# Kernel optimization log

Hardware: AMD Instinct MI355X
Metric: run time of the kernel (lower is better)

## Reference

```python
import jax, jax.numpy as jnp
import numpy as np

B, BAG, H, C = 512, 32, 1024, 53
EPS = 1e-8  # torch F.cosine_similarity denominator clamp


def setup_inputs() -> dict:
    key = jax.random.key(0)
    ks = jax.random.split(key, 5)
    return {
        "sent_reps": jax.random.normal(ks[0], (B, BAG, H), jnp.float32),
        "aug_sent_reps": jax.random.normal(ks[1], (B, BAG, H), jnp.float32),
        "rel_table": jax.random.normal(ks[2], (C, H), jnp.float32),
        "cls_w": jax.random.normal(ks[3], (C, H), jnp.float32) * 0.02,
        "cls_b": jnp.zeros((C,), jnp.float32),
        "labels": jax.random.randint(ks[4], (B,), 0, C),
        "temperature": jnp.asarray(0.1, jnp.float32),
    }


def _cl(rep, aug, bag_rep, T):
    # rep, aug: (B, bag, H); bag_rep: (B, H)
    nr = jnp.linalg.norm(rep, axis=-1)        # (B, bag)
    na = jnp.linalg.norm(aug, axis=-1)        # (B, bag)
    nb = jnp.linalg.norm(bag_rep, axis=-1)    # (B,)
    pos_sim = jnp.sum(rep * aug, axis=-1) / jnp.maximum(nr * na, EPS)  # (B, bag)
    pos = jnp.exp(pos_sim / T)
    # pair[c, j, b] = cos(rep[b, j], bag_rep[c])  -- matches torch permute/broadcast chain
    dots = jnp.einsum('bjh,ch->cjb', rep, bag_rep)               # (B, bag, B)
    denom = jnp.maximum(nb[:, None, None] * nr.T[None], EPS)      # (B, bag, B)
    pair = dots / denom
    idx = jnp.arange(rep.shape[0])
    axis_sim = pair[idx, :, idx]                                  # (B, bag): cos(rep[b,j], bag_rep[b])
    neg = jnp.exp(pair / T).sum(axis=2) - jnp.exp(axis_sim / T)   # (B, bag)
    return jnp.mean(-jnp.log(pos / (pos + neg)))


def reference(sent_reps, aug_sent_reps, rel_table, cls_w, cls_b, labels, temperature):
    # Selective attention per bag (scope slices are uniform bags of size BAG -> vectorized)
    rel = rel_table[labels]                                        # (B, H)
    scale = jnp.sqrt(jnp.asarray(H, sent_reps.dtype))
    scores = jnp.einsum('bh,bjh->bj', rel, sent_reps) / scale      # (B, bag)
    alphas = jax.nn.softmax(scores, axis=-1)
    bag_reps = jnp.einsum('bj,bjh->bh', alphas, sent_reps)         # (B, H)
    bag_out = bag_reps @ cls_w.T + cls_b                           # (B, C)  (dropout in eval = identity)
    cl_loss = _cl(sent_reps, aug_sent_reps, bag_reps, temperature)
    return bag_out, cl_loss
```

## Files before the change

kernel.cpp:

```cpp
#include <hip/hip_runtime.h>
#include <hip/hip_bf16.h>


typedef __bf16 bf16x8 __attribute__((ext_vector_type(8)));
typedef __bf16 bf16x4 __attribute__((ext_vector_type(4)));
typedef float  f32x4  __attribute__((ext_vector_type(4)));

__device__ inline float wsum(float v) {
    #pragma unroll
    for (int off = 32; off > 0; off >>= 1) v += __shfl_xor(v, off, 64);
    return v;
}

__device__ inline void gll16(const void* g, void* l) {
    __builtin_amdgcn_global_load_lds((const __attribute__((address_space(1))) void*)g,
                                     (__attribute__((address_space(3))) void*)l, 16, 0, 0);
}

__device__ inline f32x4 ntld(const float* p) {
    return __builtin_nontemporal_load((const f32x4*)p);
}

__global__ __launch_bounds__(256) void ka(
    const float* __restrict__ sent, const float* __restrict__ aug,
    const float* __restrict__ rel_table, const int* __restrict__ labels,
    __bf16* __restrict__ repb, float* __restrict__ nr, float* __restrict__ pos_sim,
    float* __restrict__ scoreg,
    const float* __restrict__ clsw, __bf16* __restrict__ cwb,
    float* __restrict__ nbsq, float* __restrict__ loss)
{
    const int t = threadIdx.x;
    if (blockIdx.x < 256) {
        const int i = blockIdx.x * 256 + t;
        cwb[i] = (i < 53 * 1024) ? (__bf16)clsw[i] : (__bf16)0.0f;
    } else if (blockIdx.x == 256) {
        nbsq[t] = 0.0f; nbsq[256 + t] = 0.0f;
        if (t == 0) *loss = 0.0f;
    }

    const int w = t >> 6, lane = t & 63;
    const int row = blockIdx.x * 4 + w;
    const int b = row >> 5;
    const size_t rbase = (size_t)row * 1024;
    const float* srow = sent + rbase;
    const float* arow = aug + rbase;
    const float* relp = rel_table + (size_t)labels[b] * 1024;

    float P = 0.f, R = 0.f, A = 0.f, D = 0.f;
    #pragma unroll
    for (int i = 0; i < 4; i++) {
        const int h = i * 256 + lane * 4;
        f32x4 v  = ntld(srow + h);
        f32x4 a  = ntld(arow + h);
        f32x4 rl = *(const f32x4*)(relp + h);
        P += v.x * rl.x + v.y * rl.y + v.z * rl.z + v.w * rl.w;
        R += v.x * v.x + v.y * v.y + v.z * v.z + v.w * v.w;
        A += a.x * a.x + a.y * a.y + a.z * a.z + a.w * a.w;
        D += v.x * a.x + v.y * a.y + v.z * a.z + v.w * a.w;
        bf16x4 vb = { (__bf16)v.x, (__bf16)v.y, (__bf16)v.z, (__bf16)v.w };
        *(bf16x4*)(repb + rbase + h) = vb;
    }
    #pragma unroll
    for (int off = 32; off > 0; off >>= 1) {
        P += __shfl_xor(P, off, 64);
        R += __shfl_xor(R, off, 64);
        A += __shfl_xor(A, off, 64);
        D += __shfl_xor(D, off, 64);
    }
    if (lane == 0) {
        scoreg[row] = P * (1.0f / 32.0f);
        float nrv = sqrtf(R), nav = sqrtf(A);
        nr[row] = nrv;
        pos_sim[row] = D / fmaxf(nrv * nav, 1e-8f);
    }
}

__global__ __launch_bounds__(256) void kb(
    const __bf16* __restrict__ repb, const float* __restrict__ scoreg,
    __bf16* __restrict__ bagb, float* __restrict__ nbsq)
{
    __shared__ float alphaS[32];
    const int b = blockIdx.x, t = threadIdx.x;
    if (t < 32) {
        float sj = scoreg[b * 32 + t];
        float m = sj;
        #pragma unroll
        for (int off = 16; off > 0; off >>= 1) m = fmaxf(m, __shfl_xor(m, off, 32));
        float e = __expf(sj - m);
        float sum = e;
        #pragma unroll
        for (int off = 16; off > 0; off >>= 1) sum += __shfl_xor(sum, off, 32);
        alphaS[t] = e / sum;
    }
    __syncthreads();

    f32x4 acc = {};
    const __bf16* base = repb + (size_t)b * 32 * 1024 + t * 4;
    #pragma unroll 8
    for (int jj = 0; jj < 32; jj++) {
        bf16x4 v = *(const bf16x4*)(base + jj * 1024);
        const float al = alphaS[jj];
        acc.x += al * (float)v.x;
        acc.y += al * (float)v.y;
        acc.z += al * (float)v.z;
        acc.w += al * (float)v.w;
    }
    bf16x4 bb = { (__bf16)acc.x, (__bf16)acc.y, (__bf16)acc.z, (__bf16)acc.w };
    *(bf16x4*)(bagb + (size_t)b * 1024 + t * 4) = bb;

    float q = acc.x * acc.x + acc.y * acc.y + acc.z * acc.z + acc.w * acc.w;
    q = wsum(q);
    if ((t & 63) == 0) atomicAdd(&nbsq[b], q);
}

__global__ __launch_bounds__(256) void k4_gemm(
    const __bf16* __restrict__ repb, const __bf16* __restrict__ bagb,
    const float* __restrict__ nr, const float* __restrict__ nbsq,
    const float* __restrict__ temp, float* __restrict__ partial, float* __restrict__ diag,
    const __bf16* __restrict__ cwb, const float* __restrict__ bias, float* __restrict__ out)
{
    __shared__ __align__(16) char smem[65536];
    const int bid = blockIdx.x;
    const int t = threadIdx.x, lane = t & 63, w = t >> 6;
    const int m = lane & 15, quad = lane >> 4;

    if (bid >= 512) {
        __bf16* Al = (__bf16*)smem;
        __bf16* Bl = (__bf16*)(smem + 8192);
        const int r0 = (bid - 512) * 64;
        f32x4 acc[4] = {};
        const int i0 = t * 8;
        const int row0 = i0 >> 5, kk0 = i0 & 31;
        const __bf16* gA = bagb + (size_t)(r0 + row0) * 1024 + kk0;
        const __bf16* gB = cwb + (size_t)row0 * 1024 + kk0;
        for (int k0 = 0; k0 < 1024; k0 += 64) {
            __syncthreads();
            gll16(gA + k0,      Al + i0);
            gll16(gA + k0 + 32, Al + 2048 + i0);
            gll16(gB + k0,      Bl + i0);
            gll16(gB + k0 + 32, Bl + 2048 + i0);
            __syncthreads();
            #pragma unroll
            for (int ks = 0; ks < 2; ks++) {
                bf16x8 a = *(const bf16x8*)(&Al[ks * 2048 + (w * 16 + m) * 32 + quad * 8]);
                #pragma unroll
                for (int n = 0; n < 4; n++) {
                    bf16x8 bf = *(const bf16x8*)(&Bl[ks * 2048 + (n * 16 + m) * 32 + quad * 8]);
                    acc[n] = __builtin_amdgcn_mfma_f32_16x16x32_bf16(a, bf, acc[n], 0, 0, 0);
                }
            }
        }
        #pragma unroll
        for (int n = 0; n < 4; n++) {
            const int c = n * 16 + m;
            if (c < 53) {
                #pragma unroll
                for (int i = 0; i < 4; i++) {
                    const int r = r0 + w * 16 + quad * 4 + i;
                    out[(size_t)r * 53 + c] = acc[n][i] + bias[c];
                }
            }
        }
        return;
    }

    __bf16* Bu0 = (__bf16*)smem;
    __bf16* Bu1 = (__bf16*)(smem + 16384);
    __bf16* Bu2 = (__bf16*)(smem + 32768);
    float (*negp)[32][128] = (float (*)[32][128])(smem + 32768);

    const int xcd = bid & 7, slot = bid >> 3;
    const int cb = slot & 3, rb = (slot >> 2) * 8 + xcd;
    const int r0 = rb * 128, c0 = cb * 128;
    const int wr0 = (w & 1) * 64, wc0 = (w >> 1) * 64;
    const int half = w & 1;

    const int swc = 8 * ((t & 3) ^ ((t >> 3) & 3));
    const size_t sOff = (size_t)(t >> 2) * 1024 + swc;
    const __bf16* pA0 = repb + (size_t)r0 * 1024 + sOff;
    const __bf16* pA1 = pA0 + 64 * 1024;
    const __bf16* pB0 = bagb + (size_t)c0 * 1024 + sOff;
    const __bf16* pB1 = pB0 + 64 * 1024;
    const int d0 = t * 8, d1 = 2048 + t * 8, d2 = 4096 + t * 8, d3 = 6144 + t * 8;

    const int rho = (m >> 1) & 3;
    const int offA = ((wr0 + m) * 4 + (quad ^ rho)) * 8;
    const int offB = 4096 + ((wc0 + m) * 4 + (quad ^ rho)) * 8;

    f32x4 acc[4][4] = {};

    #define STG(buf, s) do { const int kk_ = (s) * 32;                      \
        gll16(pA0 + kk_, (buf) + d0); gll16(pA1 + kk_, (buf) + d1);         \
        gll16(pB0 + kk_, (buf) + d2); gll16(pB1 + kk_, (buf) + d3); } while (0)

    #define CMP(buf) do { bf16x8 av_[4], bv_[4];                            \
        _Pragma("unroll") for (int i_ = 0; i_ < 4; i_++)                    \
            av_[i_] = *(const bf16x8*)((buf) + offA + i_ * 512);            \
        _Pragma("unroll") for (int n_ = 0; n_ < 4; n_++)                    \
            bv_[n_] = *(const bf16x8*)((buf) + offB + n_ * 512);            \
        _Pragma("unroll") for (int i_ = 0; i_ < 4; i_++)                    \
        _Pragma("unroll") for (int n_ = 0; n_ < 4; n_++)                    \
            acc[i_][n_] = __builtin_amdgcn_mfma_f32_16x16x32_bf16(          \
                av_[i_], bv_[n_], acc[i_][n_], 0, 0, 0); } while (0)

    #define FENCE(N) do { __builtin_amdgcn_sched_barrier(0);                \
        asm volatile("s_waitcnt vmcnt(" #N ")" ::: "memory");               \
        __builtin_amdgcn_s_barrier();                                       \
        __builtin_amdgcn_sched_barrier(0); } while (0)

    STG(Bu0, 0);
    STG(Bu1, 1);
    FENCE(4);
    #pragma unroll 1
    for (int s = 0; s < 28; s += 3) {
        STG(Bu2, s + 2); CMP(Bu0); FENCE(4);
        STG(Bu0, s + 3); CMP(Bu1); FENCE(4);
        STG(Bu1, s + 4); CMP(Bu2); FENCE(4);
    }
    CMP(Bu0);
    FENCE(0);
    CMP(Bu1);

    const float invT = 1.0f / *temp;
    float nrv[16];
    #pragma unroll
    for (int i = 0; i < 4; i++)
        #pragma unroll
        for (int g = 0; g < 4; g++)
            nrv[i * 4 + g] = nr[r0 + wr0 + i * 16 + quad * 4 + g];

    #pragma unroll
    for (int n = 0; n < 4; n++) {
        const int c_local = wc0 + n * 16 + m;
        const int cg = c0 + c_local;
        const float nbv = sqrtf(nbsq[cg]);
        #pragma unroll
        for (int i = 0; i < 2; i++) {
            #pragma unroll
            for (int g = 0; g < 4; g++) {
                const int jj = i * 16 + quad * 4 + g;
                const int rg0 = r0 + wr0 + i * 16 + quad * 4 + g;
                const int rg2 = rg0 + 32;
                float e0 = __expf(acc[i][n][g]     / fmaxf(nbv * nrv[i * 4 + g],       1e-8f) * invT);
                float e2 = __expf(acc[i + 2][n][g] / fmaxf(nbv * nrv[(i + 2) * 4 + g], 1e-8f) * invT);
                negp[half][jj][c_local] = e0 + e2;
                if ((rg0 >> 5) == cg) diag[(size_t)cg * 32 + jj] = e0;
                if ((rg2 >> 5) == cg) diag[(size_t)cg * 32 + jj] = e2;
            }
        }
    }
    __syncthreads();

    float* pout = partial + (size_t)rb * 32 * 512 + c0;
    #pragma unroll
    for (int v = 0; v < 4; v++) {
        const int idx = v * 1024 + t * 4;
        const int jj = idx >> 7, cl = idx & 127;
        f32x4 a = *(const f32x4*)(&negp[0][jj][cl]);
        f32x4 bq = *(const f32x4*)(&negp[1][jj][cl]);
        f32x4 s = a + bq;
        *(f32x4*)(pout + (size_t)jj * 512 + cl) = s;
    }
    #undef STG
    #undef CMP
    #undef FENCE
}

__global__ __launch_bounds__(256) void k5_neg(
    const float* __restrict__ partial, const float* __restrict__ diag,
    const float* __restrict__ pos_sim, const float* __restrict__ temp,
    float* __restrict__ loss)
{
    const int ct = blockIdx.x & 7, j = blockIdx.x >> 3;
    const int t = threadIdx.x, lane = t & 63, w = t >> 6;
    const int bsub = t >> 4;
    const int cidx = t & 15;
    f32x4 acc = {};
    #pragma unroll 4
    for (int r = 0; r < 8; r++) {
        const int rb = bsub * 8 + r;
        f32x4 v = *(const f32x4*)(partial + ((size_t)rb * 32 + j) * 512 + ct * 64 + cidx * 4);
        acc += v;
    }
    #pragma unroll
    for (int k = 0; k < 4; k++) {
        acc[k] += __shfl_xor(acc[k], 16, 64);
        acc[k] += __shfl_xor(acc[k], 32, 64);
    }
    __shared__ float red[4][64];
    if (lane < 16) {
        #pragma unroll
        for (int k = 0; k < 4; k++) red[w][lane * 4 + k] = acc[k];
    }
    __syncthreads();

    if (t < 64) {
        const int c = ct * 64 + t;
        float S = red[0][t] + red[1][t] + red[2][t] + red[3][t];
        S -= diag[(size_t)c * 32 + j];
        const float invT = 1.0f / *temp;
        const float lp = pos_sim[(c << 5) + j] * invT;
        float term = logf(__expf(lp) + S) - lp;
        term = wsum(term);
        if (t == 0) atomicAdd(loss, term * (1.0f / 16384.0f));
    }
}

extern "C" void kernel_launch(void* const* d_in, const int* in_sizes, int n_in,
                              void* d_out, int out_size, void* d_ws, size_t ws_size,
                              hipStream_t stream)
{
    const float* sent = (const float*)d_in[0];
    const float* aug  = (const float*)d_in[1];
    const float* rel  = (const float*)d_in[2];
    const float* clsw = (const float*)d_in[3];
    const float* clsb = (const float*)d_in[4];
    const int*   lab  = (const int*)d_in[5];
    const float* temp = (const float*)d_in[6];
    float* out = (float*)d_out;

    char* ws = (char*)d_ws;
    __bf16* bagb    = (__bf16*)(ws);
    float*  nbsq    = (float*)(ws + (1u << 20));
    float*  nr      = (float*)(ws + (1u << 20) + 64 * 1024);
    float*  pos     = (float*)(ws + (1u << 20) + 128 * 1024);
    __bf16* cwb     = (__bf16*)(ws + (1u << 20) + 192 * 1024);
    float*  scoreg  = (float*)(ws + (1u << 20) + 320 * 1024);
    float*  diag    = (float*)(ws + (2u << 20) + 64 * 1024);
    __bf16* repb    = (__bf16*)(ws + (4u << 20));
    float*  partial = (float*)(ws + (36u << 20));

    float* loss = out + 27136;

    ka     <<<4096, 256, 0, stream>>>(sent, aug, rel, lab, repb, nr, pos, scoreg,
                                      clsw, cwb, nbsq, loss);
    kb     <<<512, 256, 0, stream>>>(repb, scoreg, bagb, nbsq);
    k4_gemm<<<520, 256, 0, stream>>>(repb, bagb, nr, nbsq, temp, partial, diag,
                                     cwb, clsb, out);
    k5_neg <<<256, 256, 0, stream>>>(partial, diag, pos, temp, loss);
}
```

Measured before the change: 199.4 us.

## Fuse row-stats and bag attention kernels; use 512-thread blocks in GEMM

Merges the per-row norm/score kernel and the bag-pooling kernel into one kernel with one block per bag. Each block keeps the bf16 bag rows in LDS, so bag pooling no longer rereads repb from global memory, and nbsq is written directly instead of atomically. The score buffer and one launch go away. The GEMM kernel moves to 512 threads: the 8 waves split the columns so each wave holds half as many accumulators, and the loads are split between A and B thread halves. The trade-offs are 64KB of LDS per fused block, which limits occupancy, and only 512 blocks in the fused kernel. The small classifier GEMM path now leaves half of its threads idle.

```diff
diff --git a/kernel.cpp b/kernel.cpp
--- a/kernel.cpp
+++ b/kernel.cpp
@@ -4,6 +4,7 @@
 
 typedef __bf16 bf16x8 __attribute__((ext_vector_type(8)));
 typedef __bf16 bf16x4 __attribute__((ext_vector_type(4)));
+typedef __bf16 bf16x2 __attribute__((ext_vector_type(2)));
 typedef float  f32x4  __attribute__((ext_vector_type(4)));
 
 __device__ inline float wsum(float v) {
@@ -21,99 +22,94 @@
     return __builtin_nontemporal_load((const f32x4*)p);
 }
 
-__global__ __launch_bounds__(256) void ka(
+__global__ __launch_bounds__(512, 4) void kab(
     const float* __restrict__ sent, const float* __restrict__ aug,
     const float* __restrict__ rel_table, const int* __restrict__ labels,
     __bf16* __restrict__ repb, float* __restrict__ nr, float* __restrict__ pos_sim,
-    float* __restrict__ scoreg,
     const float* __restrict__ clsw, __bf16* __restrict__ cwb,
-    float* __restrict__ nbsq, float* __restrict__ loss)
+    __bf16* __restrict__ bagb, float* __restrict__ nbsq, float* __restrict__ loss)
 {
-    const int t = threadIdx.x;
-    if (blockIdx.x < 256) {
-        const int i = blockIdx.x * 256 + t;
+    __shared__ __align__(16) __bf16 repS[32][1024];
+    __shared__ float scoreS[32], alphaS[32], redS[8];
+    const int b = blockIdx.x, t = threadIdx.x;
+    const int w = t >> 6, lane = t & 63;
+
+    if (b < 128) {
+        const int i = b * 512 + t;
         cwb[i] = (i < 53 * 1024) ? (__bf16)clsw[i] : (__bf16)0.0f;
-    } else if (blockIdx.x == 256) {
-        nbsq[t] = 0.0f; nbsq[256 + t] = 0.0f;
-        if (t == 0) *loss = 0.0f;
-    }
-
-    const int w = t >> 6, lane = t & 63;
-    const int row = blockIdx.x * 4 + w;
-    const int b = row >> 5;
-    const size_t rbase = (size_t)row * 1024;
-    const float* srow = sent + rbase;
-    const float* arow = aug + rbase;
+        if (b == 0 && t == 0) *loss = 0.0f;
+    }
+
     const float* relp = rel_table + (size_t)labels[b] * 1024;
-
-    float P = 0.f, R = 0.f, A = 0.f, D = 0.f;
-    #pragma unroll
-    for (int i = 0; i < 4; i++) {
-        const int h = i * 256 + lane * 4;
-        f32x4 v  = ntld(srow + h);
-        f32x4 a  = ntld(arow + h);
-        f32x4 rl = *(const f32x4*)(relp + h);
-        P += v.x * rl.x + v.y * rl.y + v.z * rl.z + v.w * rl.w;
-        R += v.x * v.x + v.y * v.y + v.z * v.z + v.w * v.w;
-        A += a.x * a.x + a.y * a.y + a.z * a.z + a.w * a.w;
-        D += v.x * a.x + v.y * a.y + v.z * a.z + v.w * a.w;
-        bf16x4 vb = { (__bf16)v.x, (__bf16)v.y, (__bf16)v.z, (__bf16)v.w };
-        *(bf16x4*)(repb + rbase + h) = vb;
-    }
-    #pragma unroll
-    for (int off = 32; off > 0; off >>= 1) {
-        P += __shfl_xor(P, off, 64);
-        R += __shfl_xor(R, off, 64);
-        A += __shfl_xor(A, off, 64);
-        D += __shfl_xor(D, off, 64);
-    }
-    if (lane == 0) {
-        scoreg[row] = P * (1.0f / 32.0f);
-        float nrv = sqrtf(R), nav = sqrtf(A);
-        nr[row] = nrv;
-        pos_sim[row] = D / fmaxf(nrv * nav, 1e-8f);
-    }
-}
-
-__global__ __launch_bounds__(256) void kb(
-    const __bf16* __restrict__ repb, const float* __restrict__ scoreg,
-    __bf16* __restrict__ bagb, float* __restrict__ nbsq)
-{
-    __shared__ float alphaS[32];
-    const int b = blockIdx.x, t = threadIdx.x;
+    #pragma unroll
+    for (int rr = 0; rr < 4; rr++) {
+        const int j = w * 4 + rr;
+        const size_t rbase = ((size_t)b * 32 + j) * 1024;
+        const float* srow = sent + rbase;
+        const float* arow = aug + rbase;
+        float P = 0.f, R = 0.f, A = 0.f, D = 0.f;
+        #pragma unroll
+        for (int i = 0; i < 4; i++) {
+            const int h = i * 256 + lane * 4;
+            f32x4 v  = ntld(srow + h);
+            f32x4 a  = ntld(arow + h);
+            f32x4 rl = *(const f32x4*)(relp + h);
+            P += v.x * rl.x + v.y * rl.y + v.z * rl.z + v.w * rl.w;
+            R += v.x * v.x + v.y * v.y + v.z * v.z + v.w * v.w;
+            A += a.x * a.x + a.y * a.y + a.z * a.z + a.w * a.w;
+            D += v.x * a.x + v.y * a.y + v.z * a.z + v.w * a.w;
+            bf16x4 vb = { (__bf16)v.x, (__bf16)v.y, (__bf16)v.z, (__bf16)v.w };
+            *(bf16x4*)(&repS[j][h]) = vb;
+            *(bf16x4*)(repb + rbase + h) = vb;
+        }
+        #pragma unroll
+        for (int off = 32; off > 0; off >>= 1) {
+            P += __shfl_xor(P, off, 64);
+            R += __shfl_xor(R, off, 64);
+            A += __shfl_xor(A, off, 64);
+            D += __shfl_xor(D, off, 64);
+        }
+        if (lane == 0) {
+            scoreS[j] = P * (1.0f / 32.0f);
+            float nrv = sqrtf(R), nav = sqrtf(A);
+            nr[b * 32 + j] = nrv;
+            pos_sim[b * 32 + j] = D / fmaxf(nrv * nav, 1e-8f);
+        }
+    }
+    __syncthreads();
+
     if (t < 32) {
-        float sj = scoreg[b * 32 + t];
-        float m = sj;
-        #pragma unroll
-        for (int off = 16; off > 0; off >>= 1) m = fmaxf(m, __shfl_xor(m, off, 32));
-        float e = __expf(sj - m);
-        float sum = e;
-        #pragma unroll
-        for (int off = 16; off > 0; off >>= 1) sum += __shfl_xor(sum, off, 32);
-        alphaS[t] = e / sum;
-    }
-    __syncthreads();
-
-    f32x4 acc = {};
-    const __bf16* base = repb + (size_t)b * 32 * 1024 + t * 4;
+        float sj = scoreS[t], mx = sj;
+        #pragma unroll
+        for (int off = 16; off > 0; off >>= 1) mx = fmaxf(mx, __shfl_xor(mx, off, 32));
+        float e = __expf(sj - mx), sm = e;
+        #pragma unroll
+        for (int off = 16; off > 0; off >>= 1) sm += __shfl_xor(sm, off, 32);
+        alphaS[t] = e / sm;
+    }
+    __syncthreads();
+
+    float b0 = 0.f, b1 = 0.f;
     #pragma unroll 8
-    for (int jj = 0; jj < 32; jj++) {
-        bf16x4 v = *(const bf16x4*)(base + jj * 1024);
-        const float al = alphaS[jj];
-        acc.x += al * (float)v.x;
-        acc.y += al * (float)v.y;
-        acc.z += al * (float)v.z;
-        acc.w += al * (float)v.w;
-    }
-    bf16x4 bb = { (__bf16)acc.x, (__bf16)acc.y, (__bf16)acc.z, (__bf16)acc.w };
-    *(bf16x4*)(bagb + (size_t)b * 1024 + t * 4) = bb;
-
-    float q = acc.x * acc.x + acc.y * acc.y + acc.z * acc.z + acc.w * acc.w;
+    for (int j = 0; j < 32; j++) {
+        const float al = alphaS[j];
+        bf16x2 v = *(const bf16x2*)(&repS[j][t * 2]);
+        b0 += al * (float)v.x;
+        b1 += al * (float)v.y;
+    }
+    bf16x2 bb = { (__bf16)b0, (__bf16)b1 };
+    *(bf16x2*)(bagb + (size_t)b * 1024 + t * 2) = bb;
+
+    float q = b0 * b0 + b1 * b1;
     q = wsum(q);
-    if ((t & 63) == 0) atomicAdd(&nbsq[b], q);
-}
-
-__global__ __launch_bounds__(256) void k4_gemm(
+    if (lane == 0) redS[w] = q;
+    __syncthreads();
+    if (t == 0)
+        nbsq[b] = redS[0] + redS[1] + redS[2] + redS[3]
+                + redS[4] + redS[5] + redS[6] + redS[7];
+}
+
+__global__ __launch_bounds__(512, 4) void k4_gemm(
     const __bf16* __restrict__ repb, const __bf16* __restrict__ bagb,
     const float* __restrict__ nr, const float* __restrict__ nbsq,
     const float* __restrict__ temp, float* __restrict__ partial, float* __restrict__ diag,
@@ -129,35 +125,42 @@
         __bf16* Bl = (__bf16*)(smem + 8192);
         const int r0 = (bid - 512) * 64;
         f32x4 acc[4] = {};
-        const int i0 = t * 8;
+        const int i0 = (t & 255) * 8;
         const int row0 = i0 >> 5, kk0 = i0 & 31;
         const __bf16* gA = bagb + (size_t)(r0 + row0) * 1024 + kk0;
         const __bf16* gB = cwb + (size_t)row0 * 1024 + kk0;
+        const bool act = (t < 256);
         for (int k0 = 0; k0 < 1024; k0 += 64) {
             __syncthreads();
-            gll16(gA + k0,      Al + i0);
-            gll16(gA + k0 + 32, Al + 2048 + i0);
-            gll16(gB + k0,      Bl + i0);
-            gll16(gB + k0 + 32, Bl + 2048 + i0);
+            if (act) {
+                gll16(gA + k0,      Al + i0);
+                gll16(gA + k0 + 32, Al + 2048 + i0);
+                gll16(gB + k0,      Bl + i0);
+                gll16(gB + k0 + 32, Bl + 2048 + i0);
+            }
             __syncthreads();
-            #pragma unroll
-            for (int ks = 0; ks < 2; ks++) {
-                bf16x8 a = *(const bf16x8*)(&Al[ks * 2048 + (w * 16 + m) * 32 + quad * 8]);
+            if (act) {
                 #pragma unroll
-                for (int n = 0; n < 4; n++) {
-                    bf16x8 bf = *(const bf16x8*)(&Bl[ks * 2048 + (n * 16 + m) * 32 + quad * 8]);
-                    acc[n] = __builtin_amdgcn_mfma_f32_16x16x32_bf16(a, bf, acc[n], 0, 0, 0);
+                for (int ks = 0; ks < 2; ks++) {
+                    bf16x8 a = *(const bf16x8*)(&Al[ks * 2048 + (w * 16 + m) * 32 + quad * 8]);
+                    #pragma unroll
+                    for (int n = 0; n < 4; n++) {
+                        bf16x8 bf = *(const bf16x8*)(&Bl[ks * 2048 + (n * 16 + m) * 32 + quad * 8]);
+                        acc[n] = __builtin_amdgcn_mfma_f32_16x16x32_bf16(a, bf, acc[n], 0, 0, 0);
+                    }
                 }
             }
         }
-        #pragma unroll
-        for (int n = 0; n < 4; n++) {
-            const int c = n * 16 + m;
-            if (c < 53) {
-                #pragma unroll
-                for (int i = 0; i < 4; i++) {
-                    const int r = r0 + w * 16 + quad * 4 + i;
-                    out[(size_t)r * 53 + c] = acc[n][i] + bias[c];
+        if (act) {
+            #pragma unroll
+            for (int n = 0; n < 4; n++) {
+                const int c = n * 16 + m;
+                if (c < 53) {
+                    #pragma unroll
+                    for (int i = 0; i < 4; i++) {
+                        const int r = r0 + w * 16 + quad * 4 + i;
+                        out[(size_t)r * 53 + c] = acc[n][i] + bias[c];
+                    }
                 }
             }
         }
@@ -172,34 +175,35 @@
     const int xcd = bid & 7, slot = bid >> 3;
     const int cb = slot & 3, rb = (slot >> 2) * 8 + xcd;
     const int r0 = rb * 128, c0 = cb * 128;
-    const int wr0 = (w & 1) * 64, wc0 = (w >> 1) * 64;
+    const int wr0 = (w & 1) * 64, wc0 = (w >> 1) * 32;
     const int half = w & 1;
 
-    const int swc = 8 * ((t & 3) ^ ((t >> 3) & 3));
-    const size_t sOff = (size_t)(t >> 2) * 1024 + swc;
-    const __bf16* pA0 = repb + (size_t)r0 * 1024 + sOff;
-    const __bf16* pA1 = pA0 + 64 * 1024;
-    const __bf16* pB0 = bagb + (size_t)c0 * 1024 + sOff;
-    const __bf16* pB1 = pB0 + 64 * 1024;
-    const int d0 = t * 8, d1 = 2048 + t * 8, d2 = 4096 + t * 8, d3 = 6144 + t * 8;
+    const int tt = t & 255;
+    const bool isB = (t >= 256);
+    const int srow = tt >> 2;
+    const int scol = 8 * ((tt & 3) ^ ((srow >> 1) & 3));
+    const __bf16* g0 = (isB ? bagb + (size_t)(c0 + srow) * 1024
+                            : repb + (size_t)(r0 + srow) * 1024) + scol;
+    const __bf16* g1 = g0 + 64 * 1024;
+    const int d0 = (isB ? 4096 : 0) + tt * 8;
+    const int d1 = d0 + 2048;
 
     const int rho = (m >> 1) & 3;
     const int offA = ((wr0 + m) * 4 + (quad ^ rho)) * 8;
     const int offB = 4096 + ((wc0 + m) * 4 + (quad ^ rho)) * 8;
 
-    f32x4 acc[4][4] = {};
+    f32x4 acc[4][2] = {};
 
     #define STG(buf, s) do { const int kk_ = (s) * 32;                      \
-        gll16(pA0 + kk_, (buf) + d0); gll16(pA1 + kk_, (buf) + d1);         \
-        gll16(pB0 + kk_, (buf) + d2); gll16(pB1 + kk_, (buf) + d3); } while (0)
-
-    #define CMP(buf) do { bf16x8 av_[4], bv_[4];                            \
+        gll16(g0 + kk_, (buf) + d0); gll16(g1 + kk_, (buf) + d1); } while (0)
+
+    #define CMP(buf) do { bf16x8 av_[4], bv_[2];                            \
         _Pragma("unroll") for (int i_ = 0; i_ < 4; i_++)                    \
             av_[i_] = *(const bf16x8*)((buf) + offA + i_ * 512);            \
-        _Pragma("unroll") for (int n_ = 0; n_ < 4; n_++)                    \
+        _Pragma("unroll") for (int n_ = 0; n_ < 2; n_++)                    \
             bv_[n_] = *(const bf16x8*)((buf) + offB + n_ * 512);            \
         _Pragma("unroll") for (int i_ = 0; i_ < 4; i_++)                    \
-        _Pragma("unroll") for (int n_ = 0; n_ < 4; n_++)                    \
+        _Pragma("unroll") for (int n_ = 0; n_ < 2; n_++)                    \
             acc[i_][n_] = __builtin_amdgcn_mfma_f32_16x16x32_bf16(          \
                 av_[i_], bv_[n_], acc[i_][n_], 0, 0, 0); } while (0)
 
@@ -210,12 +214,12 @@
 
     STG(Bu0, 0);
     STG(Bu1, 1);
-    FENCE(4);
+    FENCE(2);
     #pragma unroll 1
     for (int s = 0; s < 28; s += 3) {
-        STG(Bu2, s + 2); CMP(Bu0); FENCE(4);
-        STG(Bu0, s + 3); CMP(Bu1); FENCE(4);
-        STG(Bu1, s + 4); CMP(Bu2); FENCE(4);
+        STG(Bu2, s + 2); CMP(Bu0); FENCE(2);
+        STG(Bu0, s + 3); CMP(Bu1); FENCE(2);
+        STG(Bu1, s + 4); CMP(Bu2); FENCE(2);
     }
     CMP(Bu0);
     FENCE(0);
@@ -230,7 +234,7 @@
             nrv[i * 4 + g] = nr[r0 + wr0 + i * 16 + quad * 4 + g];
 
     #pragma unroll
-    for (int n = 0; n < 4; n++) {
+    for (int n = 0; n < 2; n++) {
         const int c_local = wc0 + n * 16 + m;
         const int cg = c0 + c_local;
         const float nbv = sqrtf(nbsq[cg]);
@@ -253,8 +257,8 @@
 
     float* pout = partial + (size_t)rb * 32 * 512 + c0;
     #pragma unroll
-    for (int v = 0; v < 4; v++) {
-        const int idx = v * 1024 + t * 4;
+    for (int v = 0; v < 2; v++) {
+        const int idx = v * 2048 + t * 4;
         const int jj = idx >> 7, cl = idx & 127;
         f32x4 a = *(const f32x4*)(&negp[0][jj][cl]);
         f32x4 bq = *(const f32x4*)(&negp[1][jj][cl]);
@@ -325,17 +329,15 @@
     float*  nr      = (float*)(ws + (1u << 20) + 64 * 1024);
     float*  pos     = (float*)(ws + (1u << 20) + 128 * 1024);
     __bf16* cwb     = (__bf16*)(ws + (1u << 20) + 192 * 1024);
-    float*  scoreg  = (float*)(ws + (1u << 20) + 320 * 1024);
     float*  diag    = (float*)(ws + (2u << 20) + 64 * 1024);
     __bf16* repb    = (__bf16*)(ws + (4u << 20));
     float*  partial = (float*)(ws + (36u << 20));
 
     float* loss = out + 27136;
 
-    ka     <<<4096, 256, 0, stream>>>(sent, aug, rel, lab, repb, nr, pos, scoreg,
-                                      clsw, cwb, nbsq, loss);
-    kb     <<<512, 256, 0, stream>>>(repb, scoreg, bagb, nbsq);
-    k4_gemm<<<520, 256, 0, stream>>>(repb, bagb, nr, nbsq, temp, partial, diag,
+    kab    <<<512, 512, 0, stream>>>(sent, aug, rel, lab, repb, nr, pos,
+                                     clsw, cwb, bagb, nbsq, loss);
+    k4_gemm<<<520, 512, 0, stream>>>(repb, bagb, nr, nbsq, temp, partial, diag,
                                      cwb, clsb, out);
     k5_neg <<<256, 256, 0, stream>>>(partial, diag, pos, temp, loss);
 }
```

Result: faster. 194.7 us (-2.3%).
